# Performance work log

Measured on AMD Instinct MI355X. Metric: run time of the kernel, lower is better.

Reference implementation:

```python
import jax, jax.numpy as jnp
import numpy as np
import math

_PI = math.pi

@jax.custom_vjp
def atan_spike(h):
    # Heaviside forward, ATan surrogate (alpha=2.0) backward
    return (h >= 0).astype(h.dtype)

def _atan_fwd(h):
    return (h >= 0).astype(h.dtype), h

def _atan_bwd(h, g):
    # d/dh [ (1/pi) atan(pi*h) + 1/2 ] = 1 / (1 + (pi*h)^2)
    return (g / (1.0 + (_PI * h) ** 2),)

atan_spike.defvjp(_atan_fwd, _atan_bwd)

def plif_scan(x, alpha, v_th):
    # x: [T, ...]; PLIF: v += alpha*(x - v); spike; hard reset to 0
    a = alpha.reshape(())
    def step(v, xt):
        v = v + a * (xt - v)
        s = atan_spike(v - v_th)
        v = v * (1.0 - s)
        return v, s
    v0 = jnp.zeros_like(x[0])
    _, spikes = jax.lax.scan(step, v0, x)
    return spikes

def setup_inputs() -> dict:
    key = jax.random.key(0)
    k1, k2, k3 = jax.random.split(key, 3)
    T, B, N, D, H = 4, 8, 1024, 512, 2048
    x = jax.random.normal(k1, (T, B, N, D), dtype=jnp.float32)
    W1 = jax.random.normal(k2, (H, D), dtype=jnp.float32) * (1.0 / math.sqrt(D))
    W2 = jax.random.normal(k3, (D, H), dtype=jnp.float32) * (1.0 / math.sqrt(H))
    alpha1 = jnp.full((1,), 0.5, dtype=jnp.float32)  # 1/tau, tau=2.0
    alpha2 = jnp.full((1,), 0.5, dtype=jnp.float32)
    return {"x": x, "W1": W1, "W2": W2, "alpha1": alpha1, "alpha2": alpha2}

def reference(x, W1, W2, alpha1, alpha2):
    V_TH = 1.0
    h = jnp.einsum('tbnd,hd->tbnh', x, W1)      # fc1 (no bias)
    s1 = plif_scan(h, alpha1, V_TH)             # PLIF neuron 1
    y = jnp.einsum('tbnh,dh->tbnd', s1, W2)     # fc2 (no bias)
    s2 = plif_scan(y, alpha2, V_TH)             # PLIF neuron 2
    return s2
```

## Files before the change

### kernel.cpp

```cpp
#include <hip/hip_runtime.h>

#define T_  4
#define BN_ 8192
#define D_  512
#define H_  2048

typedef float f4 __attribute__((ext_vector_type(4)));
typedef float f32x4 __attribute__((ext_vector_type(4)));
typedef _Float16 f16x8 __attribute__((ext_vector_type(8)));

__device__ __forceinline__ void split8(const f4 u0, const f4 u1, f16x8& hi, f16x8& lo) {
#pragma unroll
    for (int i = 0; i < 4; ++i) {
        _Float16 a = (_Float16)u0[i]; hi[i]     = a; lo[i]     = (_Float16)(u0[i] - (float)a);
        _Float16 b = (_Float16)u1[i]; hi[4 + i] = b; lo[4 + i] = (_Float16)(u1[i] - (float)b);
    }
}

__device__ __forceinline__ void spikes4_to_f16(unsigned b, unsigned& lo, unsigned& hi) {
    const unsigned p0 = (b & 0xFFu) | ((b & 0xFF00u) << 8);
    const unsigned p1 = ((b >> 16) & 0xFFu) | ((b >> 8) & 0xFF0000u);
    lo = p0 * 0x3C00u;
    hi = p1 * 0x3C00u;
}

__device__ __forceinline__ void glds16(const void* g, void* l) {
    __builtin_amdgcn_global_load_lds((const __attribute__((address_space(1))) unsigned int*)g,
                                     (__attribute__((address_space(3))) unsigned int*)l, 16, 0, 0);
}

__global__ __launch_bounds__(256)
void k_split(const float* __restrict__ x, _Float16* __restrict__ xs)
{
    const int b   = blockIdx.x;
    const int t   = b & 3;
    const int k0B = (b >> 2) & 15;
    const int bnB = b >> 6;
    const int kg  = threadIdx.x & 3;
    const int row = threadIdx.x >> 2;

    const float* src = x + ((size_t)t * BN_ + bnB * 64 + row) * D_ + k0B * 32 + kg * 8;
    const f4 u0 = *(const f4*)src;
    const f4 u1 = *(const f4*)(src + 4);
    f16x8 hi, lo;
    split8(u0, u1, hi, lo);

    const size_t base = ((size_t)(bnB * 16 + k0B) * 4 + t) * 4096;
    *(f16x8*)&xs[base +        kg * 512 + row * 8] = hi;
    *(f16x8*)&xs[base + 2048 + kg * 512 + row * 8] = lo;
}

__global__ __launch_bounds__(256, 2)
void k_fc1(const _Float16* __restrict__ xs, const float* __restrict__ W1,
           const float* __restrict__ alphap, unsigned char* __restrict__ s1)
{
    __shared__ _Float16 Ab[T_][2][4][64][8];
    __shared__ _Float16 Bb[2][4][128][8];

    const int tid  = threadIdx.x;
    const int lane = tid & 63;
    const int w    = tid >> 6;
    const int wr   = (w >> 1) * 32;
    const int wc   = (w & 1) * 64;
    const int bnB  = blockIdx.x;
    const int bn0  = bnB * 64;
    const int h0   = blockIdx.y * 128;

    const int l15 = lane & 15;
    const int kgl = lane >> 4;
    const int lq  = kgl * 4;

    const int bcol = tid & 127;
    const int bkh  = tid >> 7;

    const float a1v = alphap[0];

    f32x4 acc[T_][2][4];
#pragma unroll
    for (int t = 0; t < T_; ++t)
#pragma unroll
        for (int m = 0; m < 2; ++m)
#pragma unroll
            for (int n = 0; n < 4; ++n) acc[t][m][n] = (f32x4){0.f, 0.f, 0.f, 0.f};

    const char* xbase = (const char*)xs + (size_t)bnB * 16 * 32768;
    const float* wp0  = W1 + (size_t)(h0 + bcol) * D_ + bkh * 16;

    f4 w0 = *(const f4*)wp0,       w1 = *(const f4*)(wp0 + 4);
    f4 w2 = *(const f4*)(wp0 + 8), w3 = *(const f4*)(wp0 + 12);

    for (int kb = 0; kb < 16; ++kb) {
        __syncthreads();

        const char* cb = xbase + (size_t)kb * 32768;
        _Float16* lA = &Ab[0][0][0][0][0];
#pragma unroll
        for (int i = 0; i < 8; ++i) {
            const int c = i * 4 + w;
            glds16(cb + c * 1024 + lane * 16, lA + c * 512);
        }

        {
            f16x8 hA, lA2, hB, lB;
            split8(w0, w1, hA, lA2); split8(w2, w3, hB, lB);
            *(f16x8*)&Bb[0][2 * bkh][bcol][0]     = hA;
            *(f16x8*)&Bb[0][2 * bkh + 1][bcol][0] = hB;
            *(f16x8*)&Bb[1][2 * bkh][bcol][0]     = lA2;
            *(f16x8*)&Bb[1][2 * bkh + 1][bcol][0] = lB;
        }

        if (kb < 15) {
            const float* wp = wp0 + (kb + 1) * 32;
            w0 = *(const f4*)wp;       w1 = *(const f4*)(wp + 4);
            w2 = *(const f4*)(wp + 8); w3 = *(const f4*)(wp + 12);
        }
        __syncthreads();

        f16x8 bf0[4], bf1[4];
#pragma unroll
        for (int n = 0; n < 4; ++n) {
            bf0[n] = *(const f16x8*)&Bb[0][kgl][wc + n * 16 + l15][0];
            bf1[n] = *(const f16x8*)&Bb[1][kgl][wc + n * 16 + l15][0];
        }
#pragma unroll
        for (int t = 0; t < T_; ++t)
#pragma unroll
            for (int m = 0; m < 2; ++m) {
                const f16x8 a0 = *(const f16x8*)&Ab[t][0][kgl][wr + m * 16 + l15][0];
                const f16x8 a1 = *(const f16x8*)&Ab[t][1][kgl][wr + m * 16 + l15][0];
#pragma unroll
                for (int n = 0; n < 4; ++n) {
                    acc[t][m][n] = __builtin_amdgcn_mfma_f32_16x16x32_f16(a0, bf0[n], acc[t][m][n], 0, 0, 0);
                    acc[t][m][n] = __builtin_amdgcn_mfma_f32_16x16x32_f16(a0, bf1[n], acc[t][m][n], 0, 0, 0);
                    acc[t][m][n] = __builtin_amdgcn_mfma_f32_16x16x32_f16(a1, bf0[n], acc[t][m][n], 0, 0, 0);
                }
            }
    }

#pragma unroll
    for (int m = 0; m < 2; ++m)
#pragma unroll
        for (int n = 0; n < 4; ++n)
#pragma unroll
            for (int q = 0; q < 4; ++q) {
                float v = 0.f;
#pragma unroll
                for (int t = 0; t < T_; ++t) {
                    v = v + a1v * (acc[t][m][n][q] - v);
                    const bool sp = (v >= 1.0f);
                    s1[((size_t)t * BN_ + bn0 + wr + m * 16 + lq + q) * H_ +
                       (h0 + wc + n * 16 + l15)] = sp ? (unsigned char)1 : (unsigned char)0;
                    if (sp) v = 0.f;
                }
            }
}

__global__ __launch_bounds__(256, 2)
void k_fc2(const unsigned char* __restrict__ s1, const float* __restrict__ W2,
           const float* __restrict__ alphap, float* __restrict__ out)
{
    __shared__ _Float16 A2[2][4][4][64][8];
    __shared__ _Float16 B2[2][2][4][128][8];

    const int tid  = threadIdx.x;
    const int lane = tid & 63;
    const int w    = tid >> 6;
    const int wr   = (w >> 1) * 32;
    const int wc   = (w & 1) * 64;
    const int bn0  = blockIdx.x * 64;
    const int d0   = blockIdx.y * 128;

    const int l15 = lane & 15;
    const int kgl = lane >> 4;
    const int lq  = kgl * 4;

    const int bcol = tid & 127;
    const int bkh  = tid >> 7;
    const int at   = tid >> 6;
    const int arow = lane;

    const float a2v = alphap[0];

    f32x4 acc[T_][2][4];
#pragma unroll
    for (int t = 0; t < T_; ++t)
#pragma unroll
        for (int m = 0; m < 2; ++m)
#pragma unroll
            for (int n = 0; n < 4; ++n) acc[t][m][n] = (f32x4){0.f, 0.f, 0.f, 0.f};

    const unsigned char* ap = s1 + ((size_t)at * BN_ + bn0 + arow) * H_;
    const float*         wp0 = W2 + (size_t)(d0 + bcol) * H_ + bkh * 16;

    {
        const uint4 r0 = *(const uint4*)(ap);
        const uint4 r1 = *(const uint4*)(ap + 16);
        unsigned v[8];
        spikes4_to_f16(r0.x, v[0], v[1]); spikes4_to_f16(r0.y, v[2], v[3]);
        spikes4_to_f16(r0.z, v[4], v[5]); spikes4_to_f16(r0.w, v[6], v[7]);
        *(uint4*)&A2[0][at][0][arow][0] = *(const uint4*)&v[0];
        *(uint4*)&A2[0][at][1][arow][0] = *(const uint4*)&v[4];
        spikes4_to_f16(r1.x, v[0], v[1]); spikes4_to_f16(r1.y, v[2], v[3]);
        spikes4_to_f16(r1.z, v[4], v[5]); spikes4_to_f16(r1.w, v[6], v[7]);
        *(uint4*)&A2[0][at][2][arow][0] = *(const uint4*)&v[0];
        *(uint4*)&A2[0][at][3][arow][0] = *(const uint4*)&v[4];

        const f4 w0 = *(const f4*)wp0, w1 = *(const f4*)(wp0 + 4);
        const f4 w2 = *(const f4*)(wp0 + 8), w3 = *(const f4*)(wp0 + 12);
        f16x8 hA, lA, hB, lB;
        split8(w0, w1, hA, lA); split8(w2, w3, hB, lB);
        *(f16x8*)&B2[0][0][2 * bkh][bcol][0]     = hA;
        *(f16x8*)&B2[0][0][2 * bkh + 1][bcol][0] = hB;
        *(f16x8*)&B2[0][1][2 * bkh][bcol][0]     = lA;
        *(f16x8*)&B2[0][1][2 * bkh + 1][bcol][0] = lB;
    }
    __syncthreads();

    int cur = 0;
    for (int kb = 0; kb < 64; ++kb) {
        uint4 r0, r1; f4 w0, w1, w2, w3;
        if (kb < 63) {
            r0 = *(const uint4*)(ap + (kb + 1) * 32);
            r1 = *(const uint4*)(ap + (kb + 1) * 32 + 16);
            const float* wp = wp0 + (kb + 1) * 32;
            w0 = *(const f4*)wp;       w1 = *(const f4*)(wp + 4);
            w2 = *(const f4*)(wp + 8); w3 = *(const f4*)(wp + 12);
        }

        f16x8 bf0[4], bf1[4];
#pragma unroll
        for (int n = 0; n < 4; ++n) {
            bf0[n] = *(const f16x8*)&B2[cur][0][kgl][wc + n * 16 + l15][0];
            bf1[n] = *(const f16x8*)&B2[cur][1][kgl][wc + n * 16 + l15][0];
        }
#pragma unroll
        for (int t = 0; t < T_; ++t)
#pragma unroll
            for (int m = 0; m < 2; ++m) {
                const f16x8 af = *(const f16x8*)&A2[cur][t][kgl][wr + m * 16 + l15][0];
#pragma unroll
                for (int n = 0; n < 4; ++n) {
                    acc[t][m][n] = __builtin_amdgcn_mfma_f32_16x16x32_f16(af, bf0[n], acc[t][m][n], 0, 0, 0);
                    acc[t][m][n] = __builtin_amdgcn_mfma_f32_16x16x32_f16(af, bf1[n], acc[t][m][n], 0, 0, 0);
                }
            }

        if (kb < 63) {
            unsigned v[8];
            spikes4_to_f16(r0.x, v[0], v[1]); spikes4_to_f16(r0.y, v[2], v[3]);
            spikes4_to_f16(r0.z, v[4], v[5]); spikes4_to_f16(r0.w, v[6], v[7]);
            *(uint4*)&A2[cur ^ 1][at][0][arow][0] = *(const uint4*)&v[0];
            *(uint4*)&A2[cur ^ 1][at][1][arow][0] = *(const uint4*)&v[4];
            spikes4_to_f16(r1.x, v[0], v[1]); spikes4_to_f16(r1.y, v[2], v[3]);
            spikes4_to_f16(r1.z, v[4], v[5]); spikes4_to_f16(r1.w, v[6], v[7]);
            *(uint4*)&A2[cur ^ 1][at][2][arow][0] = *(const uint4*)&v[0];
            *(uint4*)&A2[cur ^ 1][at][3][arow][0] = *(const uint4*)&v[4];

            f16x8 hA, lA, hB, lB;
            split8(w0, w1, hA, lA); split8(w2, w3, hB, lB);
            *(f16x8*)&B2[cur ^ 1][0][2 * bkh][bcol][0]     = hA;
            *(f16x8*)&B2[cur ^ 1][0][2 * bkh + 1][bcol][0] = hB;
            *(f16x8*)&B2[cur ^ 1][1][2 * bkh][bcol][0]     = lA;
            *(f16x8*)&B2[cur ^ 1][1][2 * bkh + 1][bcol][0] = lB;
        }
        __syncthreads();
        cur ^= 1;
    }

#pragma unroll
    for (int m = 0; m < 2; ++m)
#pragma unroll
        for (int n = 0; n < 4; ++n)
#pragma unroll
            for (int q = 0; q < 4; ++q) {
                float v = 0.f;
#pragma unroll
                for (int t = 0; t < T_; ++t) {
                    v = v + a2v * (acc[t][m][n][q] - v);
                    const bool sp = (v >= 1.0f);
                    out[((size_t)t * BN_ + bn0 + wr + m * 16 + lq + q) * D_ +
                        (d0 + wc + n * 16 + l15)] = sp ? 1.0f : 0.0f;
                    if (sp) v = 0.f;
                }
            }
}

extern "C" void kernel_launch(void* const* d_in, const int* in_sizes, int n_in,
                              void* d_out, int out_size, void* d_ws, size_t ws_size,
                              hipStream_t stream) {
    const float* x      = (const float*)d_in[0];
    const float* W1     = (const float*)d_in[1];
    const float* W2     = (const float*)d_in[2];
    const float* alpha1 = (const float*)d_in[3];
    const float* alpha2 = (const float*)d_in[4];
    float* out = (float*)d_out;
    unsigned char* s1 = (unsigned char*)d_ws;
    _Float16* xs = (_Float16*)d_out;

    k_split<<<dim3(8192), dim3(256), 0, stream>>>(x, xs);
    k_fc1<<<dim3(128, 16), dim3(256), 0, stream>>>(xs, W1, alpha1, s1);
    k_fc2<<<dim3(128, 4), dim3(256), 0, stream>>>(s1, W2, alpha2, out);
}
```

Measured before the change: 343.4 us.

## Pre-split W1 into fp16 hi/lo and double-buffer fc1 A tiles

Adds a kernel that converts W1 once per call into an MFMA-fragment-ordered fp16 hi/lo layout in workspace. The fc1 kernel then loads B fragments straight into registers with a one-step prefetch and double-buffers the A tiles in LDS. This removes the per-block W1 float-to-fp16 splitting, the B staging through LDS, and one barrier per k-step. In exchange it adds an extra launch, needs more workspace and LDS, and raises register pressure. It falls back to the old kernel when the workspace is too small.

After: 304.8 us. 1.13x faster.

```diff
diff --git a/kernel.cpp b/kernel.cpp
--- a/kernel.cpp
+++ b/kernel.cpp
@@ -50,12 +50,31 @@
     *(f16x8*)&xs[base + 2048 + kg * 512 + row * 8] = lo;
 }
 
+__global__ __launch_bounds__(256)
+void k_splitW(const float* __restrict__ W1, _Float16* __restrict__ w1s)
+{
+    const int gid = blockIdx.x * 256 + threadIdx.x;
+    const int col = gid & 127;
+    const int kg  = (gid >> 7) & 3;
+    const int kb  = (gid >> 9) & 15;
+    const int h0b = gid >> 13;
+
+    const float* src = W1 + (size_t)(h0b * 128 + col) * D_ + kb * 32 + kg * 8;
+    const f4 u0 = *(const f4*)src;
+    const f4 u1 = *(const f4*)(src + 4);
+    f16x8 hi, lo;
+    split8(u0, u1, hi, lo);
+
+    const size_t base = (size_t)(h0b * 16 + kb) * 8192;
+    *(f16x8*)&w1s[base +        kg * 1024 + col * 8] = hi;
+    *(f16x8*)&w1s[base + 4096 + kg * 1024 + col * 8] = lo;
+}
+
 __global__ __launch_bounds__(256, 2)
-void k_fc1(const _Float16* __restrict__ xs, const float* __restrict__ W1,
-           const float* __restrict__ alphap, unsigned char* __restrict__ s1)
+void k_fc1b(const _Float16* __restrict__ xs, const _Float16* __restrict__ w1s,
+            const float* __restrict__ alphap, unsigned char* __restrict__ s1)
 {
-    __shared__ _Float16 Ab[T_][2][4][64][8];
-    __shared__ _Float16 Bb[2][4][128][8];
+    __shared__ _Float16 Ab[2][T_][2][4][64][8];
 
     const int tid  = threadIdx.x;
     const int lane = tid & 63;
@@ -70,6 +89,117 @@
     const int kgl = lane >> 4;
     const int lq  = kgl * 4;
 
+    const float a1v = alphap[0];
+
+    f32x4 acc[T_][2][4];
+#pragma unroll
+    for (int t = 0; t < T_; ++t)
+#pragma unroll
+        for (int m = 0; m < 2; ++m)
+#pragma unroll
+            for (int n = 0; n < 4; ++n) acc[t][m][n] = (f32x4){0.f, 0.f, 0.f, 0.f};
+
+    const char* xbase = (const char*)xs + (size_t)bnB * 16 * 32768;
+    const _Float16* bl = w1s + (size_t)blockIdx.y * (16 * 8192)
+                             + (size_t)kgl * 1024 + (size_t)(wc + l15) * 8;
+
+    f16x8 bc[2][4], bn_[2][4];
+
+    {
+        _Float16* lA = &Ab[0][0][0][0][0][0];
+#pragma unroll
+        for (int i = 0; i < 8; ++i) {
+            const int c = i * 4 + w;
+            glds16(xbase + c * 1024 + lane * 16, lA + c * 512);
+        }
+#pragma unroll
+        for (int sp = 0; sp < 2; ++sp)
+#pragma unroll
+            for (int n = 0; n < 4; ++n)
+                bc[sp][n] = *(const f16x8*)(bl + sp * 4096 + n * 128);
+    }
+    __syncthreads();
+
+    int buf = 0;
+    for (int kb = 0; kb < 16; ++kb) {
+        if (kb < 15) {
+            const char* cb = xbase + (size_t)(kb + 1) * 32768;
+            _Float16* lA = &Ab[buf ^ 1][0][0][0][0][0];
+#pragma unroll
+            for (int i = 0; i < 8; ++i) {
+                const int c = i * 4 + w;
+                glds16(cb + c * 1024 + lane * 16, lA + c * 512);
+            }
+            const _Float16* bp = bl + (size_t)(kb + 1) * 8192;
+#pragma unroll
+            for (int sp = 0; sp < 2; ++sp)
+#pragma unroll
+                for (int n = 0; n < 4; ++n)
+                    bn_[sp][n] = *(const f16x8*)(bp + sp * 4096 + n * 128);
+        }
+
+#pragma unroll
+        for (int t = 0; t < T_; ++t)
+#pragma unroll
+            for (int m = 0; m < 2; ++m) {
+                const f16x8 a0 = *(const f16x8*)&Ab[buf][t][0][kgl][wr + m * 16 + l15][0];
+                const f16x8 a1 = *(const f16x8*)&Ab[buf][t][1][kgl][wr + m * 16 + l15][0];
+#pragma unroll
+                for (int n = 0; n < 4; ++n) {
+                    acc[t][m][n] = __builtin_amdgcn_mfma_f32_16x16x32_f16(a0, bc[0][n], acc[t][m][n], 0, 0, 0);
+                    acc[t][m][n] = __builtin_amdgcn_mfma_f32_16x16x32_f16(a0, bc[1][n], acc[t][m][n], 0, 0, 0);
+                    acc[t][m][n] = __builtin_amdgcn_mfma_f32_16x16x32_f16(a1, bc[0][n], acc[t][m][n], 0, 0, 0);
+                }
+            }
+
+        __syncthreads();
+        if (kb < 15) {
+#pragma unroll
+            for (int sp = 0; sp < 2; ++sp)
+#pragma unroll
+                for (int n = 0; n < 4; ++n) bc[sp][n] = bn_[sp][n];
+        }
+        buf ^= 1;
+    }
+
+#pragma unroll
+    for (int m = 0; m < 2; ++m)
+#pragma unroll
+        for (int n = 0; n < 4; ++n)
+#pragma unroll
+            for (int q = 0; q < 4; ++q) {
+                float v = 0.f;
+#pragma unroll
+                for (int t = 0; t < T_; ++t) {
+                    v = v + a1v * (acc[t][m][n][q] - v);
+                    const bool sp = (v >= 1.0f);
+                    s1[((size_t)t * BN_ + bn0 + wr + m * 16 + lq + q) * H_ +
+                       (h0 + wc + n * 16 + l15)] = sp ? (unsigned char)1 : (unsigned char)0;
+                    if (sp) v = 0.f;
+                }
+            }
+}
+
+__global__ __launch_bounds__(256, 2)
+void k_fc1(const _Float16* __restrict__ xs, const float* __restrict__ W1,
+           const float* __restrict__ alphap, unsigned char* __restrict__ s1)
+{
+    __shared__ _Float16 Ab[T_][2][4][64][8];
+    __shared__ _Float16 Bb[2][4][128][8];
+
+    const int tid  = threadIdx.x;
+    const int lane = tid & 63;
+    const int w    = tid >> 6;
+    const int wr   = (w >> 1) * 32;
+    const int wc   = (w & 1) * 64;
+    const int bnB  = blockIdx.x;
+    const int bn0  = bnB * 64;
+    const int h0   = blockIdx.y * 128;
+
+    const int l15 = lane & 15;
+    const int kgl = lane >> 4;
+    const int lq  = kgl * 4;
+
     const int bcol = tid & 127;
     const int bkh  = tid >> 7;
 
@@ -91,7 +221,6 @@
 
     for (int kb = 0; kb < 16; ++kb) {
         __syncthreads();
-
         const char* cb = xbase + (size_t)kb * 32768;
         _Float16* lA = &Ab[0][0][0][0][0];
 #pragma unroll
@@ -99,7 +228,6 @@
             const int c = i * 4 + w;
             glds16(cb + c * 1024 + lane * 16, lA + c * 512);
         }
-
         {
             f16x8 hA, lA2, hB, lB;
             split8(w0, w1, hA, lA2); split8(w2, w3, hB, lB);
@@ -108,7 +236,6 @@
             *(f16x8*)&Bb[1][2 * bkh][bcol][0]     = lA2;
             *(f16x8*)&Bb[1][2 * bkh + 1][bcol][0] = lB;
         }
-
         if (kb < 15) {
             const float* wp = wp0 + (kb + 1) * 32;
             w0 = *(const f4*)wp;       w1 = *(const f4*)(wp + 4);
@@ -294,10 +421,20 @@
     const float* alpha1 = (const float*)d_in[3];
     const float* alpha2 = (const float*)d_in[4];
     float* out = (float*)d_out;
+
     unsigned char* s1 = (unsigned char*)d_ws;
     _Float16* xs = (_Float16*)d_out;
+    const size_t S1_BYTES = (size_t)T_ * BN_ * H_;
+    const size_t W1S_BYTES = (size_t)H_ * D_ * 2 * sizeof(_Float16);
 
     k_split<<<dim3(8192), dim3(256), 0, stream>>>(x, xs);
-    k_fc1<<<dim3(128, 16), dim3(256), 0, stream>>>(xs, W1, alpha1, s1);
+
+    if (ws_size >= S1_BYTES + W1S_BYTES) {
+        _Float16* w1s = (_Float16*)((char*)d_ws + S1_BYTES);
+        k_splitW<<<dim3(512), dim3(256), 0, stream>>>(W1, w1s);
+        k_fc1b<<<dim3(128, 16), dim3(256), 0, stream>>>(xs, w1s, alpha1, s1);
+    } else {
+        k_fc1<<<dim3(128, 16), dim3(256), 0, stream>>>(xs, W1, alpha1, s1);
+    }
     k_fc2<<<dim3(128, 4), dim3(256), 0, stream>>>(s1, W2, alpha2, out);
 }
```
